# Performance work log

Hardware: AMD Instinct MI355X
Metric: run time of the kernel (lower is better)

## Reference

```python
import jax, jax.numpy as jnp
import numpy as np

EPS = 1e-5

def _conv3x3(x, w, b):
    y = jax.lax.conv_general_dilated(x, w, window_strides=(1, 1),
                                     padding=((1, 1), (1, 1)),
                                     dimension_numbers=('NCHW', 'OIHW', 'NCHW'))
    return y + b[None, :, None, None]

def _bilinear_gather(x, py, px):
    # x: [B,C,H,W]; py,px: [B,K,H,W] absolute sampling coords; zero outside image (DCN convention).
    B, C, H, W = x.shape
    Kk = py.shape[1]
    y0 = jnp.floor(py)
    x0 = jnp.floor(px)
    ly = py - y0
    lx = px - x0
    y0i = y0.astype(jnp.int32)
    x0i = x0.astype(jnp.int32)
    xf = x.reshape(B, C, H * W)

    def gather(yi, xi):
        valid = (yi >= 0) & (yi < H) & (xi >= 0) & (xi < W)
        idx = (jnp.clip(yi, 0, H - 1) * W + jnp.clip(xi, 0, W - 1)).reshape(B, -1)
        g = jax.vmap(lambda xb, ib: xb[:, ib])(xf, idx).reshape(B, C, Kk, H, W)
        return g * valid[:, None].astype(x.dtype)

    v00 = gather(y0i, x0i)
    v01 = gather(y0i, x0i + 1)
    v10 = gather(y0i + 1, x0i)
    v11 = gather(y0i + 1, x0i + 1)
    ly = ly[:, None]
    lx = lx[:, None]
    return (v00 * (1 - ly) * (1 - lx) + v01 * (1 - ly) * lx
            + v10 * ly * (1 - lx) + v11 * ly * lx)

def _shift_forward(x, w_off, b_off, w_conv, b_conv, gamma, beta, run_mean, run_var):
    B, C, H, W = x.shape
    om = _conv3x3(x, w_off, b_off)              # [B,27,H,W] offset/mask predictor
    dy = om[:, 0:18:2]                          # [B,9,H,W] per-tap y offsets
    dx = om[:, 1:18:2]                          # [B,9,H,W] per-tap x offsets
    mask = jax.nn.sigmoid(om[:, 18:27])         # [B,9,H,W] modulation (DCNv2)
    kk = jnp.arange(3, dtype=x.dtype) - 1.0     # kernel tap offsets for 3x3, dilation 1
    ky = jnp.repeat(kk, 3)                      # [9]
    kx = jnp.tile(kk, 3)                        # [9]
    hh = jnp.arange(H, dtype=x.dtype)
    ww = jnp.arange(W, dtype=x.dtype)
    py = hh[None, None, :, None] + ky[None, :, None, None] + dy
    px = ww[None, None, None, :] + kx[None, :, None, None] + dx
    s = _bilinear_gather(x, py, px) * mask[:, None]   # [B,C,9,H,W]
    Co = w_conv.shape[0]
    y = jnp.einsum('bckhw,ock->bohw', s, w_conv.reshape(Co, C, 9))
    y = y + b_conv[None, :, None, None]
    # BatchNorm2d (inference) + ReLU, then residual add
    inv = jax.lax.rsqrt(run_var + EPS)
    y = (y - run_mean[None, :, None, None]) * (inv * gamma)[None, :, None, None] + beta[None, :, None, None]
    y = jax.nn.relu(y)
    return x + y

def setup_inputs():
    key = jax.random.key(0)
    ks = jax.random.split(key, 3)
    B, C, H, W = 2, 256, 96, 96
    x = jax.random.normal(ks[0], (B, C, H, W), dtype=jnp.float32)
    w_off = jax.random.normal(ks[1], (27, C, 3, 3), dtype=jnp.float32) * 0.01
    b_off = jnp.zeros((27,), dtype=jnp.float32)
    w_conv = jax.random.normal(ks[2], (C, C, 3, 3), dtype=jnp.float32) * 0.02
    b_conv = jnp.zeros((C,), dtype=jnp.float32)
    gamma = jnp.ones((C,), dtype=jnp.float32)
    beta = jnp.zeros((C,), dtype=jnp.float32)
    run_mean = jnp.zeros((C,), dtype=jnp.float32)
    run_var = jnp.ones((C,), dtype=jnp.float32)
    return {"x": x, "w_off": w_off, "b_off": b_off, "w_conv": w_conv,
            "b_conv": b_conv, "gamma": gamma, "beta": beta,
            "run_mean": run_mean, "run_var": run_var}

def reference(x, w_off, b_off, w_conv, b_conv, gamma, beta, run_mean, run_var):
    return _shift_forward(x, w_off, b_off, w_conv, b_conv, gamma, beta, run_mean, run_var)
```

## Files before the change

### kernel.cpp

```cpp
#include <hip/hip_runtime.h>
#include <hip/hip_bf16.h>

#define H_ 96
#define W_ 96
#define HW_ 9216
#define C_ 256
#define B_ 2
#define KO_ 27
#define NPX_ 18432
#define EPS_ 1e-5f

typedef unsigned short u16;
typedef unsigned short ushort8 __attribute__((ext_vector_type(8)));
typedef short short8v __attribute__((ext_vector_type(8)));
typedef float float4v __attribute__((ext_vector_type(4)));

__device__ __forceinline__ float b2f(u16 u) {
    return __uint_as_float(((unsigned int)u) << 16);
}
__device__ __forceinline__ u16 f2b(float f) {
    __hip_bfloat16 h = __float2bfloat16(f);
    union { __hip_bfloat16 h; u16 u; } cv; cv.h = h; return cv.u;
}
__device__ __forceinline__ unsigned int pack2(float a, float b) {
    union { __hip_bfloat162 h; unsigned int u; } cv;
    cv.h = __float22bfloat162_rn(make_float2(a, b));
    return cv.u;
}
__device__ __forceinline__ void glds16(const u16* g, u16* l) {
    __builtin_amdgcn_global_load_lds(
        (const __attribute__((address_space(1))) void*)g,
        (__attribute__((address_space(3))) void*)l, 16, 0, 0);
}

__global__ __launch_bounds__(256) void prep_w_kernel(
    const float* __restrict__ w_conv, const float* __restrict__ w_off,
    const float* __restrict__ b_conv,
    const float* __restrict__ gamma, const float* __restrict__ beta,
    const float* __restrict__ rmean, const float* __restrict__ rvar,
    float* __restrict__ AB, u16* __restrict__ WQ, u16* __restrict__ WO)
{
    if (blockIdx.x == 0) {
        int o = threadIdx.x;
        float sc = gamma[o] * rsqrtf(rvar[o] + EPS_);
        AB[o] = sc;
        AB[256 + o] = beta[o] + (b_conv[o] - rmean[o]) * sc;
    }
    if (blockIdx.x < 2304) {
        int idx = blockIdx.x * 256 + threadIdx.x;
        int ch = idx >> 13;
        int o  = (idx >> 5) & 255;
        int cp = idx & 31;
        int c  = ((ch & 7) << 5) + cp;
        int k  = ch >> 3;
        WQ[idx] = f2b(w_conv[(o * C_ + c) * 9 + k]);
    } else {
        int j = (blockIdx.x - 2304) * 256 + threadIdx.x;
        int ch = j >> 10;
        int o  = (j >> 5) & 31;
        int cp = j & 31;
        int c  = ((ch & 7) << 5) + cp;
        int k  = ch >> 3;
        WO[j] = (o < KO_) ? f2b(w_off[(o * C_ + c) * 9 + k]) : (u16)0;
    }
}

__global__ __launch_bounds__(256) void xt_kernel(const float* __restrict__ x,
                                                 u16* __restrict__ XT)
{
    __shared__ u16 ls[32][100];
    int h  = blockIdx.x;
    int cg = blockIdx.y & 7;
    int b  = blockIdx.y >> 3;
    int c0 = cg * 32;
    for (int e = threadIdx.x; e < 32 * W_; e += 256) {
        int ci = e / W_, w = e % W_;
        ls[ci][w] = f2b(x[((b * C_ + c0 + ci) * H_ + h) * W_ + w]);
    }
    __syncthreads();
    for (int e = threadIdx.x; e < 32 * W_; e += 256) {
        int w = e >> 5, ci = e & 31;
        XT[((b * H_ + h) * W_ + w) * C_ + c0 + ci] = ls[ci][w];
    }
}

__global__ __launch_bounds__(256) void off_lerp_kernel(
    const u16* __restrict__ XT, const u16* __restrict__ WO,
    const float* __restrict__ b_off, u16* __restrict__ SQ)
{
    __shared__ float red[4][32][16];
    __shared__ float offv[27][16];

    const int tid = threadIdx.x;
    const int b  = blockIdx.y;
    const int p0 = blockIdx.x * 16;
    const int h  = p0 / W_;
    const int w0 = p0 % W_;

    const int wave = tid >> 6;
    const int lane = tid & 63;
    const int quad = lane >> 4;
    const int l15  = lane & 15;

    {
        const int pw = w0 + l15;
        float4v acc0 = float4v{0.f,0.f,0.f,0.f};
        float4v acc1 = float4v{0.f,0.f,0.f,0.f};
        int basec = 0; bool vld = true; int curtap = -1;
        auto set_tap = [&](int tap) {
            int py  = h + tap / 3 - 1;
            int pxl = pw + tap % 3 - 1;
            vld = ((unsigned)py < (unsigned)H_) && ((unsigned)pxl < (unsigned)W_);
            int pyc = min(max(py, 0), H_ - 1);
            int pxc = min(max(pxl, 0), W_ - 1);
            basec = ((b * H_ + pyc) * W_ + pxc) * C_ + quad * 8;
        };
        auto bload = [&](int c32) -> ushort8 {
            ushort8 v = *(const ushort8*)(XT + basec + (c32 & 7) * 32);
#pragma unroll
            for (int j = 0; j < 8; j++) v[j] = vld ? v[j] : (u16)0;
            return v;
        };
        const int c0 = wave * 18, c1 = c0 + 18;
        curtap = c0 >> 3;
        set_tap(curtap);
        ushort8 bq = bload(c0);
        short8v wa = *(const short8v*)(WO + c0 * 1024 + l15 * 32 + quad * 8);
        short8v wb = *(const short8v*)(WO + c0 * 1024 + l15 * 32 + quad * 8 + 512);
        for (int i = c0; i < c1; ++i) {
            ushort8 bc = bq;
            short8v wac = wa, wbc = wb;
            int nx = i + 1;
            if (nx < c1) {
                int t = nx >> 3;
                if (t != curtap) { set_tap(t); curtap = t; }
                bq = bload(nx);
                wa = *(const short8v*)(WO + nx * 1024 + l15 * 32 + quad * 8);
                wb = *(const short8v*)(WO + nx * 1024 + l15 * 32 + quad * 8 + 512);
            }
            union { ushort8 u; short8v s; } cb; cb.u = bc;
            acc0 = __builtin_amdgcn_mfma_f32_16x16x32_bf16(wac, cb.s, acc0, 0, 0, 0);
            acc1 = __builtin_amdgcn_mfma_f32_16x16x32_bf16(wbc, cb.s, acc1, 0, 0, 0);
        }
#pragma unroll
        for (int r = 0; r < 4; ++r) {
            red[wave][quad * 4 + r][l15]      = acc0[r];
            red[wave][16 + quad * 4 + r][l15] = acc1[r];
        }
    }
    __syncthreads();
#pragma unroll
    for (int rep = 0; rep < 2; ++rep) {
        int o  = (tid >> 4) + rep * 16;
        int px = tid & 15;
        if (o < KO_) {
            float v = red[0][o][px] + red[1][o][px] + red[2][o][px] + red[3][o][px]
                    + b_off[o];
            offv[o][px] = (o < 18) ? v : 1.f / (1.f + expf(-v));
        }
    }
    __syncthreads();

    const int j   = (tid & 3) | ((tid >> 6) << 2);
    const int px  = (tid >> 2) & 15;
    const int pw2 = w0 + px;
    const int n_base = b * HW_ + p0;

#pragma unroll 3
    for (int tap = 0; tap < 9; ++tap) {
        float dy = offv[2 * tap][px];
        float dx = offv[2 * tap + 1][px];
        float m  = offv[18 + tap][px];
        float py  = (float)(h + tap / 3 - 1) + dy;
        float pxx = (float)(pw2 + tap % 3 - 1) + dx;
        float y0f = floorf(py), x0f = floorf(pxx);
        float ly = py - y0f, lx = pxx - x0f;
        int y0 = (int)y0f, x0i = (int)x0f;
        int y1 = y0 + 1, x1 = x0i + 1;
        bool vy0 = (unsigned)y0 < (unsigned)H_;
        bool vy1 = (unsigned)y1 < (unsigned)H_;
        bool vx0 = (unsigned)x0i < (unsigned)W_;
        bool vx1 = (unsigned)x1 < (unsigned)W_;
        float fw0 = (vy0 && vx0) ? (1.f - ly) * (1.f - lx) * m : 0.f;
        float fw1 = (vy0 && vx1) ? (1.f - ly) * lx * m : 0.f;
        float fw2 = (vy1 && vx0) ? ly * (1.f - lx) * m : 0.f;
        float fw3 = (vy1 && vx1) ? ly * lx * m : 0.f;
        int y0c = min(max(y0, 0), H_ - 1), y1c = min(max(y1, 0), H_ - 1);
        int x0c = min(max(x0i, 0), W_ - 1), x1c = min(max(x1, 0), W_ - 1);
        int a00 = ((b * H_ + y0c) * W_ + x0c) * C_;
        int a01 = ((b * H_ + y0c) * W_ + x1c) * C_;
        int a10 = ((b * H_ + y1c) * W_ + x0c) * C_;
        int a11 = ((b * H_ + y1c) * W_ + x1c) * C_;
#pragma unroll
        for (int cc = 0; cc < 2; ++cc) {
            int ch = cc * 128 + j * 8;
            ushort8 v00 = *(const ushort8*)(XT + a00 + ch);
            ushort8 v01 = *(const ushort8*)(XT + a01 + ch);
            ushort8 v10 = *(const ushort8*)(XT + a10 + ch);
            ushort8 v11 = *(const ushort8*)(XT + a11 + ch);
            float v[8];
#pragma unroll
            for (int t = 0; t < 8; t++)
                v[t] = fw0 * b2f(v00[t]) + fw1 * b2f(v01[t])
                     + fw2 * b2f(v10[t]) + fw3 * b2f(v11[t]);
            uint4 sv;
            sv.x = pack2(v[0], v[1]);
            sv.y = pack2(v[2], v[3]);
            sv.z = pack2(v[4], v[5]);
            sv.w = pack2(v[6], v[7]);
            int cg = cc * 4 + (j >> 2);
            size_t base = ((size_t)(tap * 8 + cg) * NPX_ + n_base + px) * 32
                        + (j & 3) * 8;
            *(uint4*)(SQ + base) = sv;
        }
    }
}

__global__ __launch_bounds__(256) void gemm_kernel(
    const float* __restrict__ x, const u16* __restrict__ SQ,
    const u16* __restrict__ WQ, const float* __restrict__ AB,
    float* __restrict__ out)
{
    __shared__ __align__(16) u16 sA[2 * 128 * 32];
    __shared__ __align__(16) u16 sB[2 * 64 * 32];

    const int tid = threadIdx.x;
    const int wave = tid >> 6;
    const int lane = tid & 63;
    const int quad = lane >> 4;
    const int l15  = lane & 15;

    const int bid = blockIdx.x;
    const int swz = (bid & 7) * 72 + (bid >> 3);
    const int n0  = (swz >> 1) * 64;
    const int o0  = (swz & 1) * 128;

    const int wo = (wave >> 1) * 64;
    const int wp = (wave & 1) * 32;

    float4v acc[4][2];
#pragma unroll
    for (int i = 0; i < 4; i++)
#pragma unroll
        for (int jj = 0; jj < 2; jj++)
            acc[i][jj] = float4v{0.f, 0.f, 0.f, 0.f};

    const int le8 = lane * 8;

    for (int ch = 0; ch < 36; ++ch) {
#pragma unroll
        for (int i = 0; i < 4; ++i) {
            int unit = wave + i * 4;
            int cc = unit >> 3;
            const u16* g = WQ + (size_t)(ch * 2 + cc) * 8192
                         + o0 * 32 + (unit & 7) * 512 + le8;
            glds16(g, &sA[unit * 512]);
        }
#pragma unroll
        for (int i = 0; i < 2; ++i) {
            int u2 = wave + i * 4;
            int cc = u2 >> 2;
            const u16* g = SQ + ((size_t)(ch * 2 + cc) * NPX_ + n0) * 32
                         + (u2 & 3) * 512 + le8;
            glds16(g, &sB[u2 * 512]);
        }
        __syncthreads();

        short8v af[2][4], bf[2][2];
#pragma unroll
        for (int cc = 0; cc < 2; ++cc) {
#pragma unroll
            for (int mt = 0; mt < 4; ++mt)
                af[cc][mt] = *(const short8v*)
                    &sA[(cc * 128 + wo + mt * 16 + l15) * 32 + quad * 8];
#pragma unroll
            for (int nt = 0; nt < 2; ++nt)
                bf[cc][nt] = *(const short8v*)
                    &sB[(cc * 64 + wp + nt * 16 + l15) * 32 + quad * 8];
        }
#pragma unroll
        for (int cc = 0; cc < 2; ++cc)
#pragma unroll
            for (int mt = 0; mt < 4; ++mt)
#pragma unroll
                for (int nt = 0; nt < 2; ++nt)
                    acc[mt][nt] = __builtin_amdgcn_mfma_f32_16x16x32_bf16(
                        af[cc][mt], bf[cc][nt], acc[mt][nt], 0, 0, 0);
        __syncthreads();
    }

    const float* Ao = AB;
    const float* Bo = AB + 256;
    const int b    = n0 / HW_;
    const int pix0 = n0 - b * HW_ + wp;
#pragma unroll
    for (int mt = 0; mt < 4; mt++) {
#pragma unroll
        for (int nt = 0; nt < 2; nt++) {
            int pix = pix0 + nt * 16 + l15;
#pragma unroll
            for (int r = 0; r < 4; r++) {
                int o = o0 + wo + mt * 16 + quad * 4 + r;
                float v = acc[mt][nt][r] * Ao[o] + Bo[o];
                v = fmaxf(v, 0.f);
                int gi = (b * C_ + o) * HW_ + pix;
                out[gi] = x[gi] + v;
            }
        }
    }
}

extern "C" void kernel_launch(void* const* d_in, const int* in_sizes, int n_in,
                              void* d_out, int out_size, void* d_ws, size_t ws_size,
                              hipStream_t stream)
{
    (void)in_sizes; (void)n_in; (void)out_size; (void)ws_size;
    const float* x      = (const float*)d_in[0];
    const float* w_off  = (const float*)d_in[1];
    const float* b_off  = (const float*)d_in[2];
    const float* w_conv = (const float*)d_in[3];
    const float* b_conv = (const float*)d_in[4];
    const float* gamma  = (const float*)d_in[5];
    const float* beta   = (const float*)d_in[6];
    const float* rmean  = (const float*)d_in[7];
    const float* rvar   = (const float*)d_in[8];
    float* out = (float*)d_out;

    float* ws = (float*)d_ws;
    float* AB = ws;
    u16* WQ = (u16*)(AB + 512);
    u16* WO = WQ + 589824;
    u16* XT = WO + 73728;
    u16* SQ = XT + 4718592;

    prep_w_kernel<<<2592, 256, 0, stream>>>(w_conv, w_off, b_conv, gamma, beta,
                                            rmean, rvar, AB, WQ, WO);
    xt_kernel<<<dim3(96, 16), 256, 0, stream>>>(x, XT);
    off_lerp_kernel<<<dim3(576, 2), 256, 0, stream>>>(XT, WO, b_off, SQ);
    gemm_kernel<<<576, 256, 0, stream>>>(x, SQ, WQ, AB, out);
}
```

Baseline: 178.3 us.

## Fuse bilinear sampling into GEMM to eliminate sampled-column intermediate buffer

```diff
diff --git a/kernel.cpp b/kernel.cpp
--- a/kernel.cpp
+++ b/kernel.cpp
@@ -84,12 +84,11 @@
     }
 }
 
-__global__ __launch_bounds__(256) void off_lerp_kernel(
+__global__ __launch_bounds__(256) void offsets_kernel(
     const u16* __restrict__ XT, const u16* __restrict__ WO,
-    const float* __restrict__ b_off, u16* __restrict__ SQ)
+    const float* __restrict__ b_off, float* __restrict__ OFF)
 {
     __shared__ float red[4][32][16];
-    __shared__ float offv[27][16];
 
     const int tid = threadIdx.x;
     const int b  = blockIdx.y;
@@ -149,6 +148,7 @@
         }
     }
     __syncthreads();
+    const int n_base = b * HW_ + p0;
 #pragma unroll
     for (int rep = 0; rep < 2; ++rep) {
         int o  = (tid >> 4) + rep * 16;
@@ -156,48 +156,105 @@
         if (o < KO_) {
             float v = red[0][o][px] + red[1][o][px] + red[2][o][px] + red[3][o][px]
                     + b_off[o];
-            offv[o][px] = (o < 18) ? v : 1.f / (1.f + expf(-v));
-        }
+            OFF[(size_t)(n_base + px) * 32 + o] =
+                (o < 18) ? v : 1.f / (1.f + expf(-v));
+        }
+    }
+}
+
+__global__ __launch_bounds__(256) void fused_kernel(
+    const float* __restrict__ x, const u16* __restrict__ XT,
+    const float* __restrict__ OFF, const u16* __restrict__ WQ,
+    const float* __restrict__ AB, float* __restrict__ out)
+{
+    __shared__ __align__(16) u16 sA[2 * 256 * 32];
+    __shared__ __align__(16) u16 sB[2 * 32 * 32];
+    __shared__ float offv[32][32];
+
+    const int tid = threadIdx.x;
+    const int wave = tid >> 6;
+    const int lane = tid & 63;
+    const int quad = lane >> 4;
+    const int l15  = lane & 15;
+
+    const int bid = blockIdx.x;
+    const int swz = (bid & 7) * 72 + (bid >> 3);
+    const int n0  = swz * 32;
+    const int b   = n0 / HW_;
+    const int p0  = n0 - b * HW_;
+    const int h   = p0 / W_;
+    const int w0  = p0 % W_;
+
+    {
+        int px = tid >> 3, q4 = (tid & 7) * 4;
+        float4 v = *(const float4*)(OFF + (size_t)(n0 + px) * 32 + q4);
+        *(float4*)&offv[px][q4] = v;
     }
     __syncthreads();
 
-    const int j   = (tid & 3) | ((tid >> 6) << 2);
-    const int px  = (tid >> 2) & 15;
-    const int pw2 = w0 + px;
-    const int n_base = b * HW_ + p0;
-
-#pragma unroll 3
-    for (int tap = 0; tap < 9; ++tap) {
-        float dy = offv[2 * tap][px];
-        float dx = offv[2 * tap + 1][px];
-        float m  = offv[18 + tap][px];
-        float py  = (float)(h + tap / 3 - 1) + dy;
-        float pxx = (float)(pw2 + tap % 3 - 1) + dx;
-        float y0f = floorf(py), x0f = floorf(pxx);
-        float ly = py - y0f, lx = pxx - x0f;
-        int y0 = (int)y0f, x0i = (int)x0f;
-        int y1 = y0 + 1, x1 = x0i + 1;
-        bool vy0 = (unsigned)y0 < (unsigned)H_;
-        bool vy1 = (unsigned)y1 < (unsigned)H_;
-        bool vx0 = (unsigned)x0i < (unsigned)W_;
-        bool vx1 = (unsigned)x1 < (unsigned)W_;
-        float fw0 = (vy0 && vx0) ? (1.f - ly) * (1.f - lx) * m : 0.f;
-        float fw1 = (vy0 && vx1) ? (1.f - ly) * lx * m : 0.f;
-        float fw2 = (vy1 && vx0) ? ly * (1.f - lx) * m : 0.f;
-        float fw3 = (vy1 && vx1) ? ly * lx * m : 0.f;
-        int y0c = min(max(y0, 0), H_ - 1), y1c = min(max(y1, 0), H_ - 1);
-        int x0c = min(max(x0i, 0), W_ - 1), x1c = min(max(x1, 0), W_ - 1);
-        int a00 = ((b * H_ + y0c) * W_ + x0c) * C_;
-        int a01 = ((b * H_ + y0c) * W_ + x1c) * C_;
-        int a10 = ((b * H_ + y1c) * W_ + x0c) * C_;
-        int a11 = ((b * H_ + y1c) * W_ + x1c) * C_;
-#pragma unroll
-        for (int cc = 0; cc < 2; ++cc) {
-            int ch = cc * 128 + j * 8;
-            ushort8 v00 = *(const ushort8*)(XT + a00 + ch);
-            ushort8 v01 = *(const ushort8*)(XT + a01 + ch);
-            ushort8 v10 = *(const ushort8*)(XT + a10 + ch);
-            ushort8 v11 = *(const ushort8*)(XT + a11 + ch);
+    float4v acc[4][2];
+#pragma unroll
+    for (int i = 0; i < 4; i++)
+#pragma unroll
+        for (int jj = 0; jj < 2; jj++)
+            acc[i][jj] = float4v{0.f, 0.f, 0.f, 0.f};
+
+    const int le8 = lane * 8;
+    const int wo  = wave * 64;
+
+    const int ppx = tid >> 3;
+    const int pj  = tid & 7;
+    const int pcc = pj >> 2;
+    const int sboff = pcc * 1024 + ppx * 32 + (pj & 3) * 8;
+
+    float fw0 = 0.f, fw1 = 0.f, fw2 = 0.f, fw3 = 0.f;
+    int a00 = 0, a01 = 0, a10 = 0, a11 = 0;
+
+#pragma unroll 4
+    for (int ch = 0; ch < 36; ++ch) {
+        const int tap = ch >> 2, q = ch & 3;
+        if (q == 0) {
+            float dy = offv[ppx][2 * tap];
+            float dx = offv[ppx][2 * tap + 1];
+            float m  = offv[ppx][18 + tap];
+            float py  = (float)(h + tap / 3 - 1) + dy;
+            float pxx = (float)(w0 + ppx + tap % 3 - 1) + dx;
+            float y0f = floorf(py), x0f = floorf(pxx);
+            float ly = py - y0f, lx = pxx - x0f;
+            int y0 = (int)y0f, x0i = (int)x0f;
+            int y1 = y0 + 1, x1 = x0i + 1;
+            bool vy0 = (unsigned)y0 < (unsigned)H_;
+            bool vy1 = (unsigned)y1 < (unsigned)H_;
+            bool vx0 = (unsigned)x0i < (unsigned)W_;
+            bool vx1 = (unsigned)x1 < (unsigned)W_;
+            fw0 = (vy0 && vx0) ? (1.f - ly) * (1.f - lx) * m : 0.f;
+            fw1 = (vy0 && vx1) ? (1.f - ly) * lx * m : 0.f;
+            fw2 = (vy1 && vx0) ? ly * (1.f - lx) * m : 0.f;
+            fw3 = (vy1 && vx1) ? ly * lx * m : 0.f;
+            int y0c = min(max(y0, 0), H_ - 1), y1c = min(max(y1, 0), H_ - 1);
+            int x0c = min(max(x0i, 0), W_ - 1), x1c = min(max(x1, 0), W_ - 1);
+            a00 = ((b * H_ + y0c) * W_ + x0c) * C_;
+            a01 = ((b * H_ + y0c) * W_ + x1c) * C_;
+            a10 = ((b * H_ + y1c) * W_ + x0c) * C_;
+            a11 = ((b * H_ + y1c) * W_ + x1c) * C_;
+        }
+
+        const int cbase = q * 64 + pj * 8;
+        ushort8 v00 = *(const ushort8*)(XT + a00 + cbase);
+        ushort8 v01 = *(const ushort8*)(XT + a01 + cbase);
+        ushort8 v10 = *(const ushort8*)(XT + a10 + cbase);
+        ushort8 v11 = *(const ushort8*)(XT + a11 + cbase);
+
+#pragma unroll
+        for (int i = 0; i < 8; ++i) {
+            int unit = i * 4 + wave;
+            int cc = unit >> 4;
+            const u16* g = WQ + (size_t)(tap * 8 + q * 2 + cc) * 8192
+                         + (unit & 15) * 512 + le8;
+            glds16(g, &sA[unit * 512]);
+        }
+
+        {
             float v[8];
 #pragma unroll
             for (int t = 0; t < 8; t++)
@@ -208,99 +265,41 @@
             sv.y = pack2(v[2], v[3]);
             sv.z = pack2(v[4], v[5]);
             sv.w = pack2(v[6], v[7]);
-            int cg = cc * 4 + (j >> 2);
-            size_t base = ((size_t)(tap * 8 + cg) * NPX_ + n_base + px) * 32
-                        + (j & 3) * 8;
-            *(uint4*)(SQ + base) = sv;
-        }
-    }
-}
-
-__global__ __launch_bounds__(256) void gemm_kernel(
-    const float* __restrict__ x, const u16* __restrict__ SQ,
-    const u16* __restrict__ WQ, const float* __restrict__ AB,
-    float* __restrict__ out)
-{
-    __shared__ __align__(16) u16 sA[2 * 128 * 32];
-    __shared__ __align__(16) u16 sB[2 * 64 * 32];
-
-    const int tid = threadIdx.x;
-    const int wave = tid >> 6;
-    const int lane = tid & 63;
-    const int quad = lane >> 4;
-    const int l15  = lane & 15;
-
-    const int bid = blockIdx.x;
-    const int swz = (bid & 7) * 72 + (bid >> 3);
-    const int n0  = (swz >> 1) * 64;
-    const int o0  = (swz & 1) * 128;
-
-    const int wo = (wave >> 1) * 64;
-    const int wp = (wave & 1) * 32;
-
-    float4v acc[4][2];
-#pragma unroll
-    for (int i = 0; i < 4; i++)
-#pragma unroll
-        for (int jj = 0; jj < 2; jj++)
-            acc[i][jj] = float4v{0.f, 0.f, 0.f, 0.f};
-
-    const int le8 = lane * 8;
-
-    for (int ch = 0; ch < 36; ++ch) {
-#pragma unroll
-        for (int i = 0; i < 4; ++i) {
-            int unit = wave + i * 4;
-            int cc = unit >> 3;
-            const u16* g = WQ + (size_t)(ch * 2 + cc) * 8192
-                         + o0 * 32 + (unit & 7) * 512 + le8;
-            glds16(g, &sA[unit * 512]);
-        }
-#pragma unroll
-        for (int i = 0; i < 2; ++i) {
-            int u2 = wave + i * 4;
-            int cc = u2 >> 2;
-            const u16* g = SQ + ((size_t)(ch * 2 + cc) * NPX_ + n0) * 32
-                         + (u2 & 3) * 512 + le8;
-            glds16(g, &sB[u2 * 512]);
+            *(uint4*)&sB[sboff] = sv;
         }
         __syncthreads();
 
-        short8v af[2][4], bf[2][2];
 #pragma unroll
         for (int cc = 0; cc < 2; ++cc) {
+            short8v af[4], bf[2];
 #pragma unroll
             for (int mt = 0; mt < 4; ++mt)
-                af[cc][mt] = *(const short8v*)
-                    &sA[(cc * 128 + wo + mt * 16 + l15) * 32 + quad * 8];
+                af[mt] = *(const short8v*)
+                    &sA[cc * 8192 + (wo + mt * 16 + l15) * 32 + quad * 8];
 #pragma unroll
             for (int nt = 0; nt < 2; ++nt)
-                bf[cc][nt] = *(const short8v*)
-                    &sB[(cc * 64 + wp + nt * 16 + l15) * 32 + quad * 8];
-        }
-#pragma unroll
-        for (int cc = 0; cc < 2; ++cc)
+                bf[nt] = *(const short8v*)
+                    &sB[cc * 1024 + (nt * 16 + l15) * 32 + quad * 8];
 #pragma unroll
             for (int mt = 0; mt < 4; ++mt)
 #pragma unroll
                 for (int nt = 0; nt < 2; ++nt)
                     acc[mt][nt] = __builtin_amdgcn_mfma_f32_16x16x32_bf16(
-                        af[cc][mt], bf[cc][nt], acc[mt][nt], 0, 0, 0);
+                        af[mt], bf[nt], acc[mt][nt], 0, 0, 0);
+        }
         __syncthreads();
     }
 
     const float* Ao = AB;
     const float* Bo = AB + 256;
-    const int b    = n0 / HW_;
-    const int pix0 = n0 - b * HW_ + wp;
 #pragma unroll
     for (int mt = 0; mt < 4; mt++) {
 #pragma unroll
         for (int nt = 0; nt < 2; nt++) {
-            int pix = pix0 + nt * 16 + l15;
+            int pix = p0 + nt * 16 + l15;
 #pragma unroll
             for (int r = 0; r < 4; r++) {
-                int o = o0 + wo + mt * 16 + quad * 4 + r;
+                int o = wo + mt * 16 + quad * 4 + r;
                 float v = acc[mt][nt][r] * Ao[o] + Bo[o];
                 v = fmaxf(v, 0.f);
                 int gi = (b * C_ + o) * HW_ + pix;
@@ -331,11 +330,11 @@
     u16* WQ = (u16*)(AB + 512);
     u16* WO = WQ + 589824;
     u16* XT = WO + 73728;
-    u16* SQ = XT + 4718592;
+    float* OFF = (float*)(XT + 4718592);
 
     prep_w_kernel<<<2592, 256, 0, stream>>>(w_conv, w_off, b_conv, gamma, beta,
                                             rmean, rvar, AB, WQ, WO);
     xt_kernel<<<dim3(96, 16), 256, 0, stream>>>(x, XT);
-    off_lerp_kernel<<<dim3(576, 2), 256, 0, stream>>>(XT, WO, b_off, SQ);
-    gemm_kernel<<<576, 256, 0, stream>>>(x, SQ, WQ, AB, out);
-}
+    offsets_kernel<<<dim3(576, 2), 256, 0, stream>>>(XT, WO, b_off, OFF);
+    fused_kernel<<<576, 256, 0, stream>>>(x, XT, OFF, WQ, AB, out);
+}
```

Result: no change. 176.2 us (-1.2%).
